# Kernel optimization log

Measured on AMD Instinct MI355X. Metric: run time of the kernel, lower is better.

## Reference

```python
import jax, jax.numpy as jnp
import numpy as np

EPS_NORM = 1e-6  # MVLayerNorm epsilon


def _build_cayley():
    # Cl(3,0): blades as bitmasks, ordered by (grade, bitmask):
    # [1, e1, e2, e3, e12, e13, e23, e123]
    n = 3
    order = sorted(range(1 << n), key=lambda b: (bin(b).count('1'), b))
    idx = {b: i for i, b in enumerate(order)}
    C = np.zeros((8, 8, 8), dtype=np.float32)
    for a in range(8):
        for b in range(8):
            # sign from reordering basis vectors (Euclidean metric: e_i^2 = +1)
            swaps, ash = 0, a >> 1
            while ash:
                swaps += bin(ash & b).count('1')
                ash >>= 1
            C[idx[a], idx[a ^ b], idx[b]] = -1.0 if swaps % 2 else 1.0
    return C

_CAYLEY_NP = _build_cayley()
CAYLEY = jnp.asarray(_CAYLEY_NP)
# metric of each blade: scalar part of blade*blade -> [1,1,1,1,-1,-1,-1,-1]
METRIC = jnp.asarray(np.array([_CAYLEY_NP[i, 0, i] for i in range(8)], dtype=np.float32))
# blade -> grade subspace index, subspace dims [1,3,3,1]
BLADE2SUB = np.array([0, 1, 1, 1, 2, 2, 2, 3])


def mv_linear(x, w, b):
    # x: (B, in, 8); w: (out, in, 4); b: (out,) added to scalar blade only
    wb = w[:, :, BLADE2SUB]                      # (out, in, 8) per-blade weight
    y = jnp.einsum('bmi,nmi->bni', x, wb)        # (B, out, 8)
    return y.at[..., 0].add(b)


def mv_layernorm(x, a):
    # quadratic form per channel: q = sum_i g_i * x_i^2, shape (B, C, 1)
    q = jnp.einsum('bci,i,bci->bc', x, METRIC, x)[..., None]
    norm = (q * q + 1e-16) ** 0.25               # smooth sqrt(|q|)
    norm = norm.mean(axis=1, keepdims=True) + EPS_NORM  # (B, 1, 1)
    return a[None, :, None] * x / norm


def setup_inputs() -> dict:
    key = jax.random.key(0)
    ks = jax.random.split(key, 8)
    N, C_IN, C_HID, NSUB = 4096, 512, 512, 4
    s = 1.0 / np.sqrt(C_IN)
    return {
        'x': jax.random.normal(ks[0], (N, C_IN, 8), jnp.float32),
        'w1': jax.random.normal(ks[1], (C_HID, C_IN, NSUB), jnp.float32) * s,
        'b1': jax.random.normal(ks[2], (C_HID,), jnp.float32) * 0.02,
        'w2': jax.random.normal(ks[3], (C_HID, C_IN, NSUB), jnp.float32) * s,
        'b2': jax.random.normal(ks[4], (C_HID,), jnp.float32) * 0.02,
        'w3': jax.random.normal(ks[5], (C_IN, C_HID, NSUB), jnp.float32) * s,
        'b3': jax.random.normal(ks[6], (C_IN,), jnp.float32) * 0.02,
        'a_norm': jax.random.normal(ks[7], (C_IN,), jnp.float32) * 0.1 + 1.0,
    }


def reference(x, w1, b1, w2, b2, w3, b3, a_norm):
    x_l = mv_linear(x, w1, b1)                       # (N, hid, 8)
    x_r = mv_linear(x, w2, b2)                       # (N, hid, 8)
    gp = jnp.einsum('bni,ijk,bnk->bnj', x_l, CAYLEY, x_r)  # sparse Cayley product
    y = mv_linear(gp, w3, b3)                        # (N, in, 8)
    return mv_layernorm(y, a_norm)
```

## Files before the change

kernel.cpp:

```cpp
#include <hip/hip_runtime.h>
#include <hip/hip_bf16.h>
#include <cstdint>
#include <cstddef>

typedef __bf16 bf16;
typedef __bf16 bf16x4_t __attribute__((ext_vector_type(4)));
typedef __bf16 bf16x8_t __attribute__((ext_vector_type(8)));
typedef float  f32x4_t  __attribute__((ext_vector_type(4)));
typedef unsigned int u32x4_t __attribute__((ext_vector_type(4)));

#define NTOK 4096
#define CH   512
#define SLICE (NTOK*CH)
#define WSLICE (CH*CH)

__global__ __launch_bounds__(256) void k_convert_x(const float* __restrict__ x,
                                                   bf16* __restrict__ xb) {
    int p = blockIdx.x * 256 + threadIdx.x;
    const f32x4_t* x4 = (const f32x4_t*)x;
    f32x4_t v0 = x4[2*p];
    f32x4_t v1 = x4[2*p+1];
    xb[0*SLICE + p] = (bf16)v0.x;
    xb[1*SLICE + p] = (bf16)v0.y;
    xb[2*SLICE + p] = (bf16)v0.z;
    xb[3*SLICE + p] = (bf16)v0.w;
    xb[4*SLICE + p] = (bf16)v1.x;
    xb[5*SLICE + p] = (bf16)v1.y;
    xb[6*SLICE + p] = (bf16)v1.z;
    xb[7*SLICE + p] = (bf16)v1.w;
}

__global__ __launch_bounds__(256) void k_convert_w(const float* __restrict__ w,
                                                   bf16* __restrict__ wb) {
    int p = blockIdx.x * 256 + threadIdx.x;
    f32x4_t v = ((const f32x4_t*)w)[p];
    wb[0*WSLICE + p] = (bf16)v.x;
    wb[1*WSLICE + p] = (bf16)v.y;
    wb[2*WSLICE + p] = (bf16)v.z;
    wb[3*WSLICE + p] = (bf16)v.w;
}

template<int OUTF32>
__global__ __launch_bounds__(256, 2) void k_gemm(const bf16* __restrict__ Abase,
                                                 const bf16* __restrict__ Wbase,
                                                 void* __restrict__ Obase) {
    const int blade = blockIdx.z;
    const int sub = (blade == 0) ? 0 : (blade < 4) ? 1 : (blade < 7) ? 2 : 3;
    const bf16* __restrict__ A = Abase + (size_t)blade * SLICE;
    const bf16* __restrict__ B = Wbase + (size_t)sub * WSLICE;
    const int tm = blockIdx.x * 128, tn = blockIdx.y * 128;

    __shared__ __align__(128) bf16 lsA[128 * 64];
    __shared__ __align__(128) bf16 lsB[128 * 64];
    char* lsAc = (char*)lsA;
    char* lsBc = (char*)lsB;

    const int t = threadIdx.x, lane = t & 63, wid = t >> 6;
    const int waveM = (wid >> 1) * 64, waveN = (wid & 1) * 64;
    const int lrow = lane >> 3;
    const int srcc = ((lane & 7) ^ lrow) * 8;
    const int xorv = (lane & 7) << 4;
    const int kbase = (lane >> 4) * 16;

    f32x4_t acc[4][4] = {};
    u32x4_t ra[4], rb[4];

    #pragma unroll
    for (int q = 0; q < 4; ++q) {
        int row = wid * 32 + q * 8 + lrow;
        ra[q] = *(const u32x4_t*)(A + (size_t)(tm + row) * CH + srcc);
        rb[q] = *(const u32x4_t*)(B + (size_t)(tn + row) * CH + srcc);
    }

    #pragma unroll 1
    for (int kt = 0; kt < 8; ++kt) {
        __syncthreads();
        #pragma unroll
        for (int q = 0; q < 4; ++q) {
            int row = wid * 32 + q * 8 + lrow;
            *(u32x4_t*)(lsAc + row * 128 + (lane & 7) * 16) = ra[q];
            *(u32x4_t*)(lsBc + row * 128 + (lane & 7) * 16) = rb[q];
        }
        __syncthreads();
        if (kt < 7) {
            const int k0 = (kt + 1) * 64;
            #pragma unroll
            for (int q = 0; q < 4; ++q) {
                int row = wid * 32 + q * 8 + lrow;
                ra[q] = *(const u32x4_t*)(A + (size_t)(tm + row) * CH + k0 + srcc);
                rb[q] = *(const u32x4_t*)(B + (size_t)(tn + row) * CH + k0 + srcc);
            }
        }
        #pragma unroll
        for (int kk = 0; kk < 2; ++kk) {
            bf16x8_t af[4], bv[4];
            #pragma unroll
            for (int mf = 0; mf < 4; ++mf) {
                int row = waveM + mf * 16 + (lane & 15);
                af[mf] = *(const bf16x8_t*)(lsAc + row * 128 + ((kk * 64 + kbase) ^ xorv));
            }
            #pragma unroll
            for (int nf = 0; nf < 4; ++nf) {
                int row = waveN + nf * 16 + (lane & 15);
                bv[nf] = *(const bf16x8_t*)(lsBc + row * 128 + ((kk * 64 + kbase) ^ xorv));
            }
            #pragma unroll
            for (int mf = 0; mf < 4; ++mf)
                #pragma unroll
                for (int nf = 0; nf < 4; ++nf)
                    acc[mf][nf] = __builtin_amdgcn_mfma_f32_16x16x32_bf16(
                        af[mf], bv[nf], acc[mf][nf], 0, 0, 0);
        }
    }

    const int orow0 = tm + waveM + (lane >> 4) * 4;
    const int ocol  = tn + waveN + (lane & 15);
    if constexpr (OUTF32) {
        float* __restrict__ O = (float*)Obase + (size_t)blade * SLICE;
        #pragma unroll
        for (int mf = 0; mf < 4; ++mf)
            #pragma unroll
            for (int r = 0; r < 4; ++r) {
                size_t rowoff = (size_t)(orow0 + mf * 16 + r) * CH;
                #pragma unroll
                for (int nf = 0; nf < 4; ++nf)
                    O[rowoff + ocol + nf * 16] = acc[mf][nf][r];
            }
    } else {
        bf16* __restrict__ O = (bf16*)Obase + (size_t)blade * SLICE;
        #pragma unroll
        for (int mf = 0; mf < 4; ++mf)
            #pragma unroll
            for (int r = 0; r < 4; ++r) {
                size_t rowoff = (size_t)(orow0 + mf * 16 + r) * CH;
                #pragma unroll
                for (int nf = 0; nf < 4; ++nf)
                    O[rowoff + ocol + nf * 16] = (bf16)acc[mf][nf][r];
            }
    }
}

__global__ __launch_bounds__(256) void k_gp(const bf16* __restrict__ xl,
                                            const bf16* __restrict__ xr,
                                            const float* __restrict__ b1,
                                            const float* __restrict__ b2,
                                            bf16* __restrict__ gp) {
    int p = (blockIdx.x * 256 + threadIdx.x) * 4;
    float l[8][4], r[8][4], g[8][4];
    #pragma unroll
    for (int i = 0; i < 8; ++i) {
        bf16x4_t lv = *(const bf16x4_t*)(xl + (size_t)i * SLICE + p);
        bf16x4_t rv = *(const bf16x4_t*)(xr + (size_t)i * SLICE + p);
        #pragma unroll
        for (int v = 0; v < 4; ++v) { l[i][v] = (float)lv[v]; r[i][v] = (float)rv[v]; g[i][v] = 0.f; }
    }
    int n0 = p & (CH - 1);
    f32x4_t b1v = *(const f32x4_t*)(b1 + n0);
    f32x4_t b2v = *(const f32x4_t*)(b2 + n0);
    #pragma unroll
    for (int v = 0; v < 4; ++v) { l[0][v] += b1v[v]; r[0][v] += b2v[v]; }

    const int IDX[8] = {0, 1, 2, 4, 3, 5, 6, 7};
    #pragma unroll
    for (int a = 0; a < 8; ++a) {
        #pragma unroll
        for (int b = 0; b < 8; ++b) {
            int e = ((((a >> 1) ^ (a >> 2)) & b) & 1) ^ (((a >> 2) & (b >> 1)) & 1);
            int j = IDX[a ^ b], ia = IDX[a], ib = IDX[b];
            #pragma unroll
            for (int v = 0; v < 4; ++v)
                g[j][v] += e ? (-l[ia][v] * r[ib][v]) : (l[ia][v] * r[ib][v]);
        }
    }
    #pragma unroll
    for (int i = 0; i < 8; ++i) {
        bf16x4_t gv;
        #pragma unroll
        for (int v = 0; v < 4; ++v) gv[v] = (bf16)g[i][v];
        *(bf16x4_t*)(gp + (size_t)i * SLICE + p) = gv;
    }
}

__global__ __launch_bounds__(256) void k_ln(const float* __restrict__ y,
                                            const float* __restrict__ b3,
                                            const float* __restrict__ an,
                                            float* __restrict__ out) {
    int b = blockIdx.x, t = threadIdx.x;
    float yv[2][8];
    float nsum = 0.f;
    #pragma unroll
    for (int h = 0; h < 2; ++h) {
        int c = t + h * 256;
        size_t base = (size_t)b * CH + c;
        #pragma unroll
        for (int i = 0; i < 8; ++i) yv[h][i] = y[(size_t)i * SLICE + base];
        yv[h][0] += b3[c];
        float q = yv[h][0]*yv[h][0] + yv[h][1]*yv[h][1] + yv[h][2]*yv[h][2] + yv[h][3]*yv[h][3]
                - yv[h][4]*yv[h][4] - yv[h][5]*yv[h][5] - yv[h][6]*yv[h][6] - yv[h][7]*yv[h][7];
        nsum += sqrtf(sqrtf(q * q + 1e-16f));
    }
    #pragma unroll
    for (int off = 32; off; off >>= 1) nsum += __shfl_xor(nsum, off);
    __shared__ float red[4];
    if ((t & 63) == 0) red[t >> 6] = nsum;
    __syncthreads();
    float denom = (red[0] + red[1] + red[2] + red[3]) * (1.f / 512.f) + 1e-6f;
    float inv = 1.f / denom;
    #pragma unroll
    for (int h = 0; h < 2; ++h) {
        int c = t + h * 256;
        float s = an[c] * inv;
        f32x4_t o0, o1;
        o0.x = yv[h][0]*s; o0.y = yv[h][1]*s; o0.z = yv[h][2]*s; o0.w = yv[h][3]*s;
        o1.x = yv[h][4]*s; o1.y = yv[h][5]*s; o1.z = yv[h][6]*s; o1.w = yv[h][7]*s;
        size_t base8 = (size_t)((size_t)b * CH + c) * 8;
        *(f32x4_t*)(out + base8)     = o0;
        *(f32x4_t*)(out + base8 + 4) = o1;
    }
}

extern "C" void kernel_launch(void* const* d_in, const int* in_sizes, int n_in,
                              void* d_out, int out_size, void* d_ws, size_t ws_size,
                              hipStream_t stream) {
    (void)in_sizes; (void)n_in; (void)out_size; (void)ws_size;
    const float* x  = (const float*)d_in[0];
    const float* w1 = (const float*)d_in[1];
    const float* b1 = (const float*)d_in[2];
    const float* w2 = (const float*)d_in[3];
    const float* b2 = (const float*)d_in[4];
    const float* w3 = (const float*)d_in[5];
    const float* b3 = (const float*)d_in[6];
    const float* an = (const float*)d_in[7];

    char* ws = (char*)d_ws;
    bf16*  xb  = (bf16*)(ws);
    bf16*  xl  = (bf16*)(ws + 33554432);
    bf16*  xr  = (bf16*)(ws + 67108864);
    float* y   = (float*)(ws + 33554432);
    bf16*  w1b = (bf16*)(ws + 100663296);
    bf16*  w2b = (bf16*)(ws + 102760448);
    bf16*  w3b = (bf16*)(ws + 104857600);

    k_convert_x<<<SLICE / 256, 256, 0, stream>>>(x, xb);
    k_convert_w<<<WSLICE / 256, 256, 0, stream>>>(w1, w1b);
    k_convert_w<<<WSLICE / 256, 256, 0, stream>>>(w2, w2b);
    k_convert_w<<<WSLICE / 256, 256, 0, stream>>>(w3, w3b);

    dim3 gg(NTOK / 128, CH / 128, 8);
    k_gemm<0><<<gg, 256, 0, stream>>>(xb, w1b, (void*)xl);
    k_gemm<0><<<gg, 256, 0, stream>>>(xb, w2b, (void*)xr);
    k_gp<<<SLICE / 4 / 256, 256, 0, stream>>>(xl, xr, b1, b2, xb );
    k_gemm<1><<<gg, 256, 0, stream>>>(xb, w3b, (void*)y);
    k_ln<<<NTOK, 256, 0, stream>>>(y, b3, an, (float*)d_out);
}
```

Before: 254.2 us.

## Fuse dual GEMMs, use direct global-to-LDS loads, store y as bf16

Merges the two left/right projection GEMMs into one kernel that shares the A tile and keeps two accumulator sets. Operand staging now uses global_load_lds direct copies instead of register prefetch. The three weight conversions become one launch, and the final GEMM output drops to bf16, which the layernorm reads as vectorized pairs. The aim is less A-matrix traffic, fewer launches and less output bandwidth. In exchange it doubles accumulator registers, which may hurt occupancy, drops the register-prefetch overlap with compute, and adds bf16 rounding error on y.

```diff
diff --git a/kernel.cpp b/kernel.cpp
--- a/kernel.cpp
+++ b/kernel.cpp
@@ -4,8 +4,10 @@
 #include <cstddef>
 
 typedef __bf16 bf16;
+typedef __bf16 bf16x2_t __attribute__((ext_vector_type(2)));
 typedef __bf16 bf16x4_t __attribute__((ext_vector_type(4)));
 typedef __bf16 bf16x8_t __attribute__((ext_vector_type(8)));
+typedef float  f32x2_t  __attribute__((ext_vector_type(2)));
 typedef float  f32x4_t  __attribute__((ext_vector_type(4)));
 typedef unsigned int u32x4_t __attribute__((ext_vector_type(4)));
 
@@ -13,6 +15,14 @@
 #define CH   512
 #define SLICE (NTOK*CH)
 #define WSLICE (CH*CH)
+
+#define AS1 __attribute__((address_space(1)))
+#define AS3 __attribute__((address_space(3)))
+
+__device__ __forceinline__ void gl_lds16(const void* g, void* l) {
+    __builtin_amdgcn_global_load_lds((const AS1 unsigned int*)g,
+                                     (AS3 unsigned int*)l, 16, 0, 0);
+}
 
 __global__ __launch_bounds__(256) void k_convert_x(const float* __restrict__ x,
                                                    bf16* __restrict__ xb) {
@@ -30,9 +40,15 @@
     xb[7*SLICE + p] = (bf16)v1.w;
 }
 
-__global__ __launch_bounds__(256) void k_convert_w(const float* __restrict__ w,
-                                                   bf16* __restrict__ wb) {
+__global__ __launch_bounds__(256) void k_convert_w(const float* __restrict__ w1,
+                                                   const float* __restrict__ w2,
+                                                   const float* __restrict__ w3,
+                                                   bf16* __restrict__ w1b,
+                                                   bf16* __restrict__ w2b,
+                                                   bf16* __restrict__ w3b) {
     int p = blockIdx.x * 256 + threadIdx.x;
+    const float* w = (blockIdx.y == 0) ? w1 : (blockIdx.y == 1) ? w2 : w3;
+    bf16* wb       = (blockIdx.y == 0) ? w1b : (blockIdx.y == 1) ? w2b : w3b;
     f32x4_t v = ((const f32x4_t*)w)[p];
     wb[0*WSLICE + p] = (bf16)v.x;
     wb[1*WSLICE + p] = (bf16)v.y;
@@ -40,83 +56,97 @@
     wb[3*WSLICE + p] = (bf16)v.w;
 }
 
-template<int OUTF32>
+template<int DUAL>
 __global__ __launch_bounds__(256, 2) void k_gemm(const bf16* __restrict__ Abase,
-                                                 const bf16* __restrict__ Wbase,
-                                                 void* __restrict__ Obase) {
+                                                 const bf16* __restrict__ W1base,
+                                                 const bf16* __restrict__ W2base,
+                                                 bf16* __restrict__ O1base,
+                                                 bf16* __restrict__ O2base) {
     const int blade = blockIdx.z;
     const int sub = (blade == 0) ? 0 : (blade < 4) ? 1 : (blade < 7) ? 2 : 3;
-    const bf16* __restrict__ A = Abase + (size_t)blade * SLICE;
-    const bf16* __restrict__ B = Wbase + (size_t)sub * WSLICE;
+    const bf16* A  = Abase + (size_t)blade * SLICE;
+    const bf16* B1 = W1base + (size_t)sub * WSLICE;
+    const bf16* B2 = W2base + (size_t)sub * WSLICE;
     const int tm = blockIdx.x * 128, tn = blockIdx.y * 128;
 
-    __shared__ __align__(128) bf16 lsA[128 * 64];
-    __shared__ __align__(128) bf16 lsB[128 * 64];
-    char* lsAc = (char*)lsA;
-    char* lsBc = (char*)lsB;
+    __shared__ __align__(1024) bf16 lsA[128 * 64];
+    __shared__ __align__(1024) bf16 lsB1[128 * 64];
+    __shared__ __align__(1024) bf16 lsB2[DUAL ? 128 * 64 : 64];
+    char* lsAc  = (char*)lsA;
+    char* lsB1c = (char*)lsB1;
+    char* lsB2c = (char*)lsB2;
 
     const int t = threadIdx.x, lane = t & 63, wid = t >> 6;
     const int waveM = (wid >> 1) * 64, waveN = (wid & 1) * 64;
-    const int lrow = lane >> 3;
-    const int srcc = ((lane & 7) ^ lrow) * 8;
-    const int xorv = (lane & 7) << 4;
+
+    const int srow = wid * 32 + (lane >> 3);
+    const int sswz = ((lane & 7) ^ (srow & 7)) * 8;
+    const bf16* Ag  = A  + (size_t)(tm + srow) * CH + sswz;
+    const bf16* B1g = B1 + (size_t)(tn + srow) * CH + sswz;
+    const bf16* B2g = B2 + (size_t)(tn + srow) * CH + sswz;
+    const int ldsq = wid * 4096;
+
+    const int xorv  = (lane & 7) << 4;
     const int kbase = (lane >> 4) * 16;
 
-    f32x4_t acc[4][4] = {};
-    u32x4_t ra[4], rb[4];
-
-    #pragma unroll
-    for (int q = 0; q < 4; ++q) {
-        int row = wid * 32 + q * 8 + lrow;
-        ra[q] = *(const u32x4_t*)(A + (size_t)(tm + row) * CH + srcc);
-        rb[q] = *(const u32x4_t*)(B + (size_t)(tn + row) * CH + srcc);
-    }
+    f32x4_t accL[4][4] = {};
+    f32x4_t accR[4][4] = {};
 
     #pragma unroll 1
     for (int kt = 0; kt < 8; ++kt) {
         __syncthreads();
+        const int k0 = kt * 64;
         #pragma unroll
         for (int q = 0; q < 4; ++q) {
-            int row = wid * 32 + q * 8 + lrow;
-            *(u32x4_t*)(lsAc + row * 128 + (lane & 7) * 16) = ra[q];
-            *(u32x4_t*)(lsBc + row * 128 + (lane & 7) * 16) = rb[q];
+            gl_lds16(Ag  + (size_t)q * 8 * CH + k0, lsAc  + ldsq + q * 1024);
+            gl_lds16(B1g + (size_t)q * 8 * CH + k0, lsB1c + ldsq + q * 1024);
+            if constexpr (DUAL)
+                gl_lds16(B2g + (size_t)q * 8 * CH + k0, lsB2c + ldsq + q * 1024);
         }
         __syncthreads();
-        if (kt < 7) {
-            const int k0 = (kt + 1) * 64;
-            #pragma unroll
-            for (int q = 0; q < 4; ++q) {
-                int row = wid * 32 + q * 8 + lrow;
-                ra[q] = *(const u32x4_t*)(A + (size_t)(tm + row) * CH + k0 + srcc);
-                rb[q] = *(const u32x4_t*)(B + (size_t)(tn + row) * CH + k0 + srcc);
-            }
-        }
         #pragma unroll
         for (int kk = 0; kk < 2; ++kk) {
-            bf16x8_t af[4], bv[4];
+            const int koff = kk * 64 + kbase;
+            bf16x8_t af[4], b1v[4], b2v[4];
             #pragma unroll
             for (int mf = 0; mf < 4; ++mf) {
                 int row = waveM + mf * 16 + (lane & 15);
-                af[mf] = *(const bf16x8_t*)(lsAc + row * 128 + ((kk * 64 + kbase) ^ xorv));
+                af[mf] = *(const bf16x8_t*)(lsAc + row * 128 + (koff ^ xorv));
             }
             #pragma unroll
             for (int nf = 0; nf < 4; ++nf) {
                 int row = waveN + nf * 16 + (lane & 15);
-                bv[nf] = *(const bf16x8_t*)(lsBc + row * 128 + ((kk * 64 + kbase) ^ xorv));
+                b1v[nf] = *(const bf16x8_t*)(lsB1c + row * 128 + (koff ^ xorv));
+                if constexpr (DUAL)
+                    b2v[nf] = *(const bf16x8_t*)(lsB2c + row * 128 + (koff ^ xorv));
             }
             #pragma unroll
             for (int mf = 0; mf < 4; ++mf)
                 #pragma unroll
-                for (int nf = 0; nf < 4; ++nf)
-                    acc[mf][nf] = __builtin_amdgcn_mfma_f32_16x16x32_bf16(
-                        af[mf], bv[nf], acc[mf][nf], 0, 0, 0);
+                for (int nf = 0; nf < 4; ++nf) {
+                    accL[mf][nf] = __builtin_amdgcn_mfma_f32_16x16x32_bf16(
+                        af[mf], b1v[nf], accL[mf][nf], 0, 0, 0);
+                    if constexpr (DUAL)
+                        accR[mf][nf] = __builtin_amdgcn_mfma_f32_16x16x32_bf16(
+                            af[mf], b2v[nf], accR[mf][nf], 0, 0, 0);
+                }
         }
     }
 
     const int orow0 = tm + waveM + (lane >> 4) * 4;
     const int ocol  = tn + waveN + (lane & 15);
-    if constexpr (OUTF32) {
-        float* __restrict__ O = (float*)Obase + (size_t)blade * SLICE;
+    bf16* O1 = O1base + (size_t)blade * SLICE;
+    #pragma unroll
+    for (int mf = 0; mf < 4; ++mf)
+        #pragma unroll
+        for (int r = 0; r < 4; ++r) {
+            size_t rowoff = (size_t)(orow0 + mf * 16 + r) * CH;
+            #pragma unroll
+            for (int nf = 0; nf < 4; ++nf)
+                O1[rowoff + ocol + nf * 16] = (bf16)accL[mf][nf][r];
+        }
+    if constexpr (DUAL) {
+        bf16* O2 = O2base + (size_t)blade * SLICE;
         #pragma unroll
         for (int mf = 0; mf < 4; ++mf)
             #pragma unroll
@@ -124,18 +154,7 @@
                 size_t rowoff = (size_t)(orow0 + mf * 16 + r) * CH;
                 #pragma unroll
                 for (int nf = 0; nf < 4; ++nf)
-                    O[rowoff + ocol + nf * 16] = acc[mf][nf][r];
-            }
-    } else {
-        bf16* __restrict__ O = (bf16*)Obase + (size_t)blade * SLICE;
-        #pragma unroll
-        for (int mf = 0; mf < 4; ++mf)
-            #pragma unroll
-            for (int r = 0; r < 4; ++r) {
-                size_t rowoff = (size_t)(orow0 + mf * 16 + r) * CH;
-                #pragma unroll
-                for (int nf = 0; nf < 4; ++nf)
-                    O[rowoff + ocol + nf * 16] = (bf16)acc[mf][nf][r];
+                    O2[rowoff + ocol + nf * 16] = (bf16)accR[mf][nf][r];
             }
     }
 }
@@ -181,20 +200,25 @@
     }
 }
 
-__global__ __launch_bounds__(256) void k_ln(const float* __restrict__ y,
+__global__ __launch_bounds__(256) void k_ln(const bf16* __restrict__ y,
                                             const float* __restrict__ b3,
                                             const float* __restrict__ an,
                                             float* __restrict__ out) {
     int b = blockIdx.x, t = threadIdx.x;
+    int c0 = t * 2;
+    size_t base = (size_t)b * CH + c0;
     float yv[2][8];
+    #pragma unroll
+    for (int i = 0; i < 8; ++i) {
+        bf16x2_t v = *(const bf16x2_t*)(y + (size_t)i * SLICE + base);
+        yv[0][i] = (float)v[0];
+        yv[1][i] = (float)v[1];
+    }
+    f32x2_t b3v = *(const f32x2_t*)(b3 + c0);
     float nsum = 0.f;
     #pragma unroll
     for (int h = 0; h < 2; ++h) {
-        int c = t + h * 256;
-        size_t base = (size_t)b * CH + c;
-        #pragma unroll
-        for (int i = 0; i < 8; ++i) yv[h][i] = y[(size_t)i * SLICE + base];
-        yv[h][0] += b3[c];
+        yv[h][0] += b3v[h];
         float q = yv[h][0]*yv[h][0] + yv[h][1]*yv[h][1] + yv[h][2]*yv[h][2] + yv[h][3]*yv[h][3]
                 - yv[h][4]*yv[h][4] - yv[h][5]*yv[h][5] - yv[h][6]*yv[h][6] - yv[h][7]*yv[h][7];
         nsum += sqrtf(sqrtf(q * q + 1e-16f));
@@ -206,17 +230,18 @@
     __syncthreads();
     float denom = (red[0] + red[1] + red[2] + red[3]) * (1.f / 512.f) + 1e-6f;
     float inv = 1.f / denom;
+    f32x2_t anv = *(const f32x2_t*)(an + c0);
+    float out16[16];
     #pragma unroll
     for (int h = 0; h < 2; ++h) {
-        int c = t + h * 256;
-        float s = an[c] * inv;
-        f32x4_t o0, o1;
-        o0.x = yv[h][0]*s; o0.y = yv[h][1]*s; o0.z = yv[h][2]*s; o0.w = yv[h][3]*s;
-        o1.x = yv[h][4]*s; o1.y = yv[h][5]*s; o1.z = yv[h][6]*s; o1.w = yv[h][7]*s;
-        size_t base8 = (size_t)((size_t)b * CH + c) * 8;
-        *(f32x4_t*)(out + base8)     = o0;
-        *(f32x4_t*)(out + base8 + 4) = o1;
-    }
+        float s = anv[h] * inv;
+        #pragma unroll
+        for (int i = 0; i < 8; ++i) out16[h * 8 + i] = yv[h][i] * s;
+    }
+    size_t base8 = base * 8;
+    #pragma unroll
+    for (int j = 0; j < 4; ++j)
+        *(f32x4_t*)(out + base8 + j * 4) = *(f32x4_t*)(out16 + j * 4);
 }
 
 extern "C" void kernel_launch(void* const* d_in, const int* in_sizes, int n_in,
@@ -236,20 +261,18 @@
     bf16*  xb  = (bf16*)(ws);
     bf16*  xl  = (bf16*)(ws + 33554432);
     bf16*  xr  = (bf16*)(ws + 67108864);
-    float* y   = (float*)(ws + 33554432);
+    bf16*  yb  = (bf16*)(ws + 33554432);
     bf16*  w1b = (bf16*)(ws + 100663296);
     bf16*  w2b = (bf16*)(ws + 102760448);
     bf16*  w3b = (bf16*)(ws + 104857600);
 
     k_convert_x<<<SLICE / 256, 256, 0, stream>>>(x, xb);
-    k_convert_w<<<WSLICE / 256, 256, 0, stream>>>(w1, w1b);
-    k_convert_w<<<WSLICE / 256, 256, 0, stream>>>(w2, w2b);
-    k_convert_w<<<WSLICE / 256, 256, 0, stream>>>(w3, w3b);
+    dim3 gw(WSLICE / 256, 3);
+    k_convert_w<<<gw, 256, 0, stream>>>(w1, w2, w3, w1b, w2b, w3b);
 
     dim3 gg(NTOK / 128, CH / 128, 8);
-    k_gemm<0><<<gg, 256, 0, stream>>>(xb, w1b, (void*)xl);
-    k_gemm<0><<<gg, 256, 0, stream>>>(xb, w2b, (void*)xr);
+    k_gemm<1><<<gg, 256, 0, stream>>>(xb, w1b, w2b, xl, xr);
     k_gp<<<SLICE / 4 / 256, 256, 0, stream>>>(xl, xr, b1, b2, xb );
-    k_gemm<1><<<gg, 256, 0, stream>>>(xb, w3b, (void*)y);
-    k_ln<<<NTOK, 256, 0, stream>>>(y, b3, an, (float*)d_out);
-}
+    k_gemm<0><<<gg, 256, 0, stream>>>(xb, w3b, w3b, yb, yb);
+    k_ln<<<NTOK, 256, 0, stream>>>(yb, b3, an, (float*)d_out);
+}
```

New measurement: 244.6 us. 1.04x faster.
